# Optimization experiments

Measured on AMD Instinct MI355X. Metric: run time of the kernel, lower is better.

Reference implementation:

```python
import jax, jax.numpy as jnp
import numpy as np


def _unfold(x, k, pad, stride):
    # torch F.unfold: [B,C,H,W] -> [B, C*k*k, L] with (C, kh, kw) channel-major ordering
    B, C, H, W = x.shape
    xp = jnp.pad(x, ((0, 0), (0, 0), (pad, pad), (pad, pad)))
    oh = (H + 2 * pad - k) // stride + 1
    ow = (W + 2 * pad - k) // stride + 1
    rows = (jnp.arange(oh) * stride)[:, None] + jnp.arange(k)[None, :]  # [oh,k]
    cols = (jnp.arange(ow) * stride)[:, None] + jnp.arange(k)[None, :]  # [ow,k]
    p = xp[:, :, rows][:, :, :, :, cols]          # [B,C,oh,k,ow,k]
    p = p.transpose(0, 1, 3, 5, 2, 4)             # [B,C,k,k,oh,ow]
    return p.reshape(B, C * k * k, oh * ow)


def _fold(p, out_hw, k, pad, stride):
    # torch F.fold: overlap-add of patches [B, C*k*k, L] -> [B,C,H,W]
    B = p.shape[0]
    C = p.shape[1] // (k * k)
    H, W = out_hw
    oh = (H + 2 * pad - k) // stride + 1
    ow = (W + 2 * pad - k) // stride + 1
    p = p.reshape(B, C, k, k, oh, ow).transpose(0, 1, 4, 2, 5, 3)  # [B,C,oh,k,ow,k]
    rows = (jnp.arange(oh) * stride)[:, None] + jnp.arange(k)[None, :]  # [oh,k]
    cols = (jnp.arange(ow) * stride)[:, None] + jnp.arange(k)[None, :]  # [ow,k]
    out = jnp.zeros((B, C, H + 2 * pad, W + 2 * pad), p.dtype)
    out = out.at[:, :, rows[:, :, None, None], cols[None, None, :, :]].add(p)
    return out[:, :, pad:pad + H, pad:pad + W]


def _bis_gather(unf, idx):
    # torch.gather along dim=2 with per-batch index broadcast over channels
    return jnp.take_along_axis(unf, idx[:, None, :], axis=2)


def setup_inputs() -> dict:
    key = jax.random.key(0)
    k1, k2, k3, k4 = jax.random.split(key, 4)
    B, H, W = 4, 96, 96
    L = H * W
    return {
        "R_lv2_star_arg": jax.random.randint(k1, (B, L), 0, L, dtype=jnp.int64 if jax.config.jax_enable_x64 else jnp.int32).astype(jnp.int32),
        "lrsr_lv2": jax.random.normal(k2, (B, 64, H, W), dtype=jnp.float32),
        "ref_lv1": jax.random.normal(k3, (B, 64, 2 * H, 2 * W), dtype=jnp.float32),
        "ref_lv2": jax.random.normal(k4, (B, 128, H, W), dtype=jnp.float32),
    }


def reference(R_lv2_star_arg, lrsr_lv2, ref_lv1, ref_lv2):
    H, W = lrsr_lv2.shape[2], lrsr_lv2.shape[3]
    ref_lv2_unfold = _unfold(ref_lv2, 3, 1, 1)   # [B, C2*9, H*W]
    ref_lv1_unfold = _unfold(ref_lv1, 6, 2, 2)   # [B, C1*36, H*W]
    T_lv2_unfold = _bis_gather(ref_lv2_unfold, R_lv2_star_arg)
    T_lv1_unfold = _bis_gather(ref_lv1_unfold, R_lv2_star_arg)
    T_lv2 = _fold(T_lv2_unfold, (H, W), 3, 1, 1) / 9.0
    T_lv1 = _fold(T_lv1_unfold, (2 * H, 2 * W), 6, 2, 2) / 9.0
    return (T_lv2, T_lv1)
```

## Files before the change

kernel.cpp:

```cpp
#include <hip/hip_runtime.h>


typedef float f2 __attribute__((ext_vector_type(2)));
typedef float f4 __attribute__((ext_vector_type(4)));

#define NINE_INV (1.0f / 9.0f)
#define ZCELL 9216u

__device__ __forceinline__ unsigned cvt_pk_bf16(float a, float b) {
    unsigned r;
    asm("v_cvt_pk_bf16_f32 %0, %1, %2" : "=v"(r) : "v"(a), "v"(b));
    return r;
}
__device__ __forceinline__ f2 up2(unsigned w) {
    f2 r;
    r.x = __builtin_bit_cast(float, w << 16);
    r.y = __builtin_bit_cast(float, w & 0xffff0000u);
    return r;
}
template <typename T> __device__ __forceinline__ T ntload(const T* p) {
    return __builtin_nontemporal_load(p);
}
template <typename T> __device__ __forceinline__ void ntstore(T* p, T v) {
    __builtin_nontemporal_store(v, p);
}

__global__ __launch_bounds__(256) void table_kernel(
    const int* __restrict__ idx, uint4* __restrict__ tabA,
    unsigned short* __restrict__ tabB)
{
    int g = blockIdx.x * 256 + threadIdx.x;
    int b = g / 9216;
    int u = g - b * 9216;
    const int* idxb = idx + b * 9216;
    int r = u / 96, t = u - 96 * r;
    unsigned e[9];
#pragma unroll
    for (int i = 0; i < 3; ++i) {
        int oy = r - 1 + i;
        bool oyv = (unsigned)oy < 96u;
#pragma unroll
        for (int j = 0; j < 3; ++j) {
            int ox = t - 1 + j;
            bool pv = oyv & ((unsigned)ox < 96u);
            int jv = idxb[pv ? oy * 96 + ox : 0];
            int jy = jv / 96, jx = jv - 96 * jy;
            int ysh = jy + 1 - i, xsh = jx + 1 - j;
            bool sv = pv & ((unsigned)ysh < 96u) & ((unsigned)xsh < 96u);
            e[i * 3 + j] = sv ? (unsigned)(ysh * 96 + xsh) : ZCELL;
        }
    }
    uint4 w;
    w.x = e[0] | (e[1] << 16);
    w.y = e[2] | (e[3] << 16);
    w.z = e[4] | (e[5] << 16);
    w.w = e[6] | (e[7] << 16);
    tabA[g] = w;
    tabB[g] = (unsigned short)e[8];
}

template <bool TAB>
__global__ __launch_bounds__(512, 4) void transfer_kernel(
    const int* __restrict__ idx,
    const float* __restrict__ ref1,
    const float* __restrict__ ref2,
    const uint4* __restrict__ tabA,
    const unsigned short* __restrict__ tabB,
    float* __restrict__ out)
{
    __shared__ __align__(16) unsigned s2[18436];
    const int tid = threadIdx.x;
    const int bid = blockIdx.x;
    const int b = bid & 3;

    if (tid < 4) s2[18432 + tid] = 0;

    const uint4* tA = tabA + b * 9216;
    const unsigned short* tB = tabB + b * 9216;
    const int* idxb = idx + b * 9216;
    const f2 nv = {NINE_INV, NINE_INV};

    auto inline_cells = [&](int u, unsigned* e) {
        int r = u / 96, t = u - 96 * r;
#pragma unroll
        for (int i = 0; i < 3; ++i) {
            int oy = r - 1 + i;
            bool oyv = (unsigned)oy < 96u;
#pragma unroll
            for (int j = 0; j < 3; ++j) {
                int ox = t - 1 + j;
                bool pv = oyv & ((unsigned)ox < 96u);
                int jv = idxb[pv ? oy * 96 + ox : 0];
                int jy = jv / 96, jx = jv - 96 * jy;
                int ysh = jy + 1 - i, xsh = jx + 1 - j;
                bool sv = pv & ((unsigned)ysh < 96u) & ((unsigned)xsh < 96u);
                e[i * 3 + j] = sv ? (unsigned)(ysh * 96 + xsh) : ZCELL;
            }
        }
    };

    auto do_taps = [&](const unsigned* cw, unsigned c8, f2& a0, f2& a1) {
#pragma unroll
        for (int q = 0; q < 4; ++q) {
            unsigned lo = cw[q] & 0xffffu, hi = cw[q] >> 16;
            uint2 wa = *(const uint2*)((const char*)s2 + (lo << 3));
            uint2 wb = *(const uint2*)((const char*)s2 + (hi << 3));
            a0 += up2(wa.x); a1 += up2(wa.y);
            a0 += up2(wb.x); a1 += up2(wb.y);
        }
        uint2 wc = *(const uint2*)((const char*)s2 + (c8 << 3));
        a0 += up2(wc.x); a1 += up2(wc.y);
    };

    if (bid < 256) {
        const int q = (bid >> 2) & 1, c0 = (bid >> 3) * 2;
        const float* g0 = ref1 + (size_t)(b * 64 + c0) * 36864;

        for (int u2 = tid; u2 < 4608; u2 += 512) {
            int ysh = u2 / 48, xsh0 = 2 * (u2 - 48 * ysh);
            const float* gp = g0 + (size_t)(2 * ysh + q) * 192 + 2 * xsh0;
            f4 va = ntload((const f4*)gp);
            f4 vb = ntload((const f4*)(gp + 36864));
            uint4 w;
            w.x = cvt_pk_bf16(va.x, va.y); w.y = cvt_pk_bf16(vb.x, vb.y);
            w.z = cvt_pk_bf16(va.z, va.w); w.w = cvt_pk_bf16(vb.z, vb.w);
            *(uint4*)(s2 + 4 * u2) = w;
        }
        __syncthreads();

        float* ob = out + 4718592 + (size_t)(b * 64 + c0) * 36864;

        uint4 cA; unsigned cB;
        if (TAB) { cA = tA[tid]; cB = tB[tid]; }
        int u = tid;
#pragma unroll 2
        for (int k = 0; k < 18; ++k) {
            uint4 nA = cA; unsigned nB = cB;
            if (TAB && k < 17) { nA = tA[u + 512]; nB = tB[u + 512]; }
            unsigned cw[4];
            unsigned c8;
            if (TAB) {
                cw[0] = cA.x; cw[1] = cA.y; cw[2] = cA.z; cw[3] = cA.w; c8 = cB;
            } else {
                unsigned e[9];
                inline_cells(u, e);
                cw[0] = e[0] | (e[1] << 16); cw[1] = e[2] | (e[3] << 16);
                cw[2] = e[4] | (e[5] << 16); cw[3] = e[6] | (e[7] << 16);
                c8 = e[8];
            }
            f2 a0 = {0.f, 0.f}, a1 = {0.f, 0.f};
            do_taps(cw, c8, a0, a1);
            a0 *= nv; a1 *= nv;
            int r = u / 96, t = u - 96 * r;
            float* op = ob + (size_t)(2 * r + q) * 192 + 2 * t;
            ntstore((f2*)op, a0);
            ntstore((f2*)(op + 36864), a1);
            u += 512; cA = nA; cB = nB;
        }
    } else {
        const int r2 = bid - 256;
        const int grp = (r2 >> 2) & 31, h = (r2 >> 7) & 1;
        const int c0 = grp * 4;
        const float* g0 = ref2 + (size_t)(b * 128 + c0) * 9216;

        for (int u2 = tid; u2 < 4608; u2 += 512) {
            f2 p0 = ntload((const f2*)(g0 + 2 * u2));
            f2 p1 = ntload((const f2*)(g0 + 9216 + 2 * u2));
            f2 p2 = ntload((const f2*)(g0 + 2 * 9216 + 2 * u2));
            f2 p3 = ntload((const f2*)(g0 + 3 * 9216 + 2 * u2));
            uint4 w;
            w.x = cvt_pk_bf16(p0.x, p1.x); w.y = cvt_pk_bf16(p2.x, p3.x);
            w.z = cvt_pk_bf16(p0.y, p1.y); w.w = cvt_pk_bf16(p2.y, p3.y);
            *(uint4*)(s2 + 4 * u2) = w;
        }
        __syncthreads();

        float* ob = out + (size_t)(b * 128 + c0) * 9216;

        const int u0 = h * 4608;
        uint4 cA; unsigned cB;
        if (TAB) { cA = tA[u0 + tid]; cB = tB[u0 + tid]; }
        int u = u0 + tid;
#pragma unroll 2
        for (int k = 0; k < 9; ++k) {
            uint4 nA = cA; unsigned nB = cB;
            if (TAB && k < 8) { nA = tA[u + 512]; nB = tB[u + 512]; }
            unsigned cw[4];
            unsigned c8;
            if (TAB) {
                cw[0] = cA.x; cw[1] = cA.y; cw[2] = cA.z; cw[3] = cA.w; c8 = cB;
            } else {
                unsigned e[9];
                inline_cells(u, e);
                cw[0] = e[0] | (e[1] << 16); cw[1] = e[2] | (e[3] << 16);
                cw[2] = e[4] | (e[5] << 16); cw[3] = e[6] | (e[7] << 16);
                c8 = e[8];
            }
            f2 a0 = {0.f, 0.f}, a1 = {0.f, 0.f};
            do_taps(cw, c8, a0, a1);
            a0 *= nv; a1 *= nv;
            float* op = ob + u;
            ntstore(op, a0.x);            ntstore(op + 9216, a0.y);
            ntstore(op + 2 * 9216, a1.x); ntstore(op + 3 * 9216, a1.y);
            u += 512; cA = nA; cB = nB;
        }
    }
}

extern "C" void kernel_launch(void* const* d_in, const int* in_sizes, int n_in,
                              void* d_out, int out_size, void* d_ws, size_t ws_size,
                              hipStream_t stream) {
    const int*   idx  = (const int*)d_in[0];
    const float* ref1 = (const float*)d_in[2];
    const float* ref2 = (const float*)d_in[3];
    float* outp = (float*)d_out;

    uint4* tabA = (uint4*)d_ws;
    unsigned short* tabB = (unsigned short*)((char*)d_ws + (size_t)4 * 9216 * 16);

    const size_t need = (size_t)4 * 9216 * 16 + (size_t)4 * 9216 * 2;
    if (ws_size >= need) {
        hipLaunchKernelGGL(table_kernel, dim3(144), dim3(256), 0, stream,
                           idx, tabA, tabB);
        hipLaunchKernelGGL(transfer_kernel<true>, dim3(512), dim3(512), 0, stream,
                           idx, ref1, ref2, tabA, tabB, outp);
    } else {
        hipLaunchKernelGGL(transfer_kernel<false>, dim3(512), dim3(512), 0, stream,
                           idx, ref1, ref2, tabA, tabB, outp);
    }
}
```

Measured before the change: 27.69 us.

## Process more channels per block with wider LDS gathers and 1024-thread blocks

Each block now stages twice as many channels in shared memory (4 for the lv1 path, 8 for the lv2 path) as packed bf16, so one 16-byte LDS gather per tap serves more channels. The index-table reads per output position are therefore amortized over more channels. Blocks are doubled to 1024 threads, and the grid is halved to 256 blocks. The shared-memory footprint doubles to about 147KB per block, which limits blocks per CU, and the smaller grid may leave part of the GPU idle.

```diff
diff --git a/kernel.cpp b/kernel.cpp
--- a/kernel.cpp
+++ b/kernel.cpp
@@ -60,7 +60,7 @@
 }
 
 template <bool TAB>
-__global__ __launch_bounds__(512, 4) void transfer_kernel(
+__global__ __launch_bounds__(1024, 4) void transfer_kernel(
     const int* __restrict__ idx,
     const float* __restrict__ ref1,
     const float* __restrict__ ref2,
@@ -68,20 +68,21 @@
     const unsigned short* __restrict__ tabB,
     float* __restrict__ out)
 {
-    __shared__ __align__(16) unsigned s2[18436];
+    __shared__ __align__(16) unsigned s4[36868];
     const int tid = threadIdx.x;
     const int bid = blockIdx.x;
+
+    if (tid < 4) s4[36864 + tid] = 0;
+
     const int b = bid & 3;
-
-    if (tid < 4) s2[18432 + tid] = 0;
-
     const uint4* tA = tabA + b * 9216;
     const unsigned short* tB = tabB + b * 9216;
     const int* idxb = idx + b * 9216;
     const f2 nv = {NINE_INV, NINE_INV};
 
-    auto inline_cells = [&](int u, unsigned* e) {
+    auto make_cells = [&](int u, uint4& A, unsigned& B) {
         int r = u / 96, t = u - 96 * r;
+        unsigned e[9];
 #pragma unroll
         for (int i = 0; i < 3; ++i) {
             int oy = r - 1 + i;
@@ -97,34 +98,37 @@
                 e[i * 3 + j] = sv ? (unsigned)(ysh * 96 + xsh) : ZCELL;
             }
         }
+        A.x = e[0] | (e[1] << 16); A.y = e[2] | (e[3] << 16);
+        A.z = e[4] | (e[5] << 16); A.w = e[6] | (e[7] << 16);
+        B = e[8];
     };
 
-    auto do_taps = [&](const unsigned* cw, unsigned c8, f2& a0, f2& a1) {
-#pragma unroll
-        for (int q = 0; q < 4; ++q) {
-            unsigned lo = cw[q] & 0xffffu, hi = cw[q] >> 16;
-            uint2 wa = *(const uint2*)((const char*)s2 + (lo << 3));
-            uint2 wb = *(const uint2*)((const char*)s2 + (hi << 3));
-            a0 += up2(wa.x); a1 += up2(wa.y);
-            a0 += up2(wb.x); a1 += up2(wb.y);
-        }
-        uint2 wc = *(const uint2*)((const char*)s2 + (c8 << 3));
-        a0 += up2(wc.x); a1 += up2(wc.y);
+    auto gather4 = [&](uint4 cA, unsigned cB, f2& a0, f2& a1, f2& a2, f2& a3) {
+#define TAP(c) { uint4 w = *(const uint4*)((const char*)s4 + ((unsigned)(c) << 4)); \
+                 a0 += up2(w.x); a1 += up2(w.y); a2 += up2(w.z); a3 += up2(w.w); }
+        TAP(cA.x & 0xffffu); TAP(cA.x >> 16);
+        TAP(cA.y & 0xffffu); TAP(cA.y >> 16);
+        TAP(cA.z & 0xffffu); TAP(cA.z >> 16);
+        TAP(cA.w & 0xffffu); TAP(cA.w >> 16);
+        TAP(cB);
+#undef TAP
     };
 
-    if (bid < 256) {
-        const int q = (bid >> 2) & 1, c0 = (bid >> 3) * 2;
+    if (bid < 128) {
+        const int q = (bid >> 2) & 1, c0 = (bid >> 3) * 4;
         const float* g0 = ref1 + (size_t)(b * 64 + c0) * 36864;
 
-        for (int u2 = tid; u2 < 4608; u2 += 512) {
-            int ysh = u2 / 48, xsh0 = 2 * (u2 - 48 * ysh);
-            const float* gp = g0 + (size_t)(2 * ysh + q) * 192 + 2 * xsh0;
-            f4 va = ntload((const f4*)gp);
-            f4 vb = ntload((const f4*)(gp + 36864));
+        for (int u2 = tid; u2 < 9216; u2 += 1024) {
+            int ysh = u2 / 96, xsh = u2 - 96 * ysh;
+            const float* gp = g0 + (size_t)(2 * ysh + q) * 192 + 2 * xsh;
+            f2 v0 = ntload((const f2*)gp);
+            f2 v1 = ntload((const f2*)(gp + 36864));
+            f2 v2 = ntload((const f2*)(gp + 2 * 36864));
+            f2 v3 = ntload((const f2*)(gp + 3 * 36864));
             uint4 w;
-            w.x = cvt_pk_bf16(va.x, va.y); w.y = cvt_pk_bf16(vb.x, vb.y);
-            w.z = cvt_pk_bf16(va.z, va.w); w.w = cvt_pk_bf16(vb.z, vb.w);
-            *(uint4*)(s2 + 4 * u2) = w;
+            w.x = cvt_pk_bf16(v0.x, v0.y); w.y = cvt_pk_bf16(v1.x, v1.y);
+            w.z = cvt_pk_bf16(v2.x, v2.y); w.w = cvt_pk_bf16(v3.x, v3.y);
+            *(uint4*)(s4 + 4 * u2) = w;
         }
         __syncthreads();
 
@@ -134,75 +138,77 @@
         if (TAB) { cA = tA[tid]; cB = tB[tid]; }
         int u = tid;
 #pragma unroll 2
-        for (int k = 0; k < 18; ++k) {
+        for (int k = 0; k < 9; ++k) {
             uint4 nA = cA; unsigned nB = cB;
-            if (TAB && k < 17) { nA = tA[u + 512]; nB = tB[u + 512]; }
-            unsigned cw[4];
-            unsigned c8;
-            if (TAB) {
-                cw[0] = cA.x; cw[1] = cA.y; cw[2] = cA.z; cw[3] = cA.w; c8 = cB;
-            } else {
-                unsigned e[9];
-                inline_cells(u, e);
-                cw[0] = e[0] | (e[1] << 16); cw[1] = e[2] | (e[3] << 16);
-                cw[2] = e[4] | (e[5] << 16); cw[3] = e[6] | (e[7] << 16);
-                c8 = e[8];
-            }
-            f2 a0 = {0.f, 0.f}, a1 = {0.f, 0.f};
-            do_taps(cw, c8, a0, a1);
-            a0 *= nv; a1 *= nv;
+            if (TAB && k < 8) { nA = tA[u + 1024]; nB = tB[u + 1024]; }
+            if (!TAB) make_cells(u, cA, cB);
+            f2 a0 = {0.f, 0.f}, a1 = {0.f, 0.f}, a2 = {0.f, 0.f}, a3 = {0.f, 0.f};
+            gather4(cA, cB, a0, a1, a2, a3);
+            a0 *= nv; a1 *= nv; a2 *= nv; a3 *= nv;
             int r = u / 96, t = u - 96 * r;
             float* op = ob + (size_t)(2 * r + q) * 192 + 2 * t;
             ntstore((f2*)op, a0);
             ntstore((f2*)(op + 36864), a1);
-            u += 512; cA = nA; cB = nB;
+            ntstore((f2*)(op + 2 * 36864), a2);
+            ntstore((f2*)(op + 3 * 36864), a3);
+            u += 1024; cA = nA; cB = nB;
         }
     } else {
-        const int r2 = bid - 256;
-        const int grp = (r2 >> 2) & 31, h = (r2 >> 7) & 1;
-        const int c0 = grp * 4;
+        const int r2 = bid - 128;
+        const int grp = (r2 >> 2) & 15, h = (r2 >> 6) & 1;
+        const int c0 = grp * 8;
         const float* g0 = ref2 + (size_t)(b * 128 + c0) * 9216;
 
-        for (int u2 = tid; u2 < 4608; u2 += 512) {
-            f2 p0 = ntload((const f2*)(g0 + 2 * u2));
-            f2 p1 = ntload((const f2*)(g0 + 9216 + 2 * u2));
-            f2 p2 = ntload((const f2*)(g0 + 2 * 9216 + 2 * u2));
-            f2 p3 = ntload((const f2*)(g0 + 3 * 9216 + 2 * u2));
-            uint4 w;
-            w.x = cvt_pk_bf16(p0.x, p1.x); w.y = cvt_pk_bf16(p2.x, p3.x);
-            w.z = cvt_pk_bf16(p0.y, p1.y); w.w = cvt_pk_bf16(p2.y, p3.y);
-            *(uint4*)(s2 + 4 * u2) = w;
+        for (int p = tid; p < 4608; p += 1024) {
+            const float* gp = g0 + 2 * p;
+            f2 v0 = ntload((const f2*)gp);
+            f2 v1 = ntload((const f2*)(gp + 9216));
+            f2 v2 = ntload((const f2*)(gp + 2 * 9216));
+            f2 v3 = ntload((const f2*)(gp + 3 * 9216));
+            f2 v4 = ntload((const f2*)(gp + 4 * 9216));
+            f2 v5 = ntload((const f2*)(gp + 5 * 9216));
+            f2 v6 = ntload((const f2*)(gp + 6 * 9216));
+            f2 v7 = ntload((const f2*)(gp + 7 * 9216));
+            uint4 wa, wb;
+            wa.x = cvt_pk_bf16(v0.x, v1.x); wa.y = cvt_pk_bf16(v2.x, v3.x);
+            wa.z = cvt_pk_bf16(v4.x, v5.x); wa.w = cvt_pk_bf16(v6.x, v7.x);
+            wb.x = cvt_pk_bf16(v0.y, v1.y); wb.y = cvt_pk_bf16(v2.y, v3.y);
+            wb.z = cvt_pk_bf16(v4.y, v5.y); wb.w = cvt_pk_bf16(v6.y, v7.y);
+            *(uint4*)(s4 + 8 * p) = wa;
+            *(uint4*)(s4 + 8 * p + 4) = wb;
         }
         __syncthreads();
 
         float* ob = out + (size_t)(b * 128 + c0) * 9216;
-
         const int u0 = h * 4608;
-        uint4 cA; unsigned cB;
-        if (TAB) { cA = tA[u0 + tid]; cB = tB[u0 + tid]; }
-        int u = u0 + tid;
-#pragma unroll 2
-        for (int k = 0; k < 9; ++k) {
-            uint4 nA = cA; unsigned nB = cB;
-            if (TAB && k < 8) { nA = tA[u + 512]; nB = tB[u + 512]; }
-            unsigned cw[4];
-            unsigned c8;
-            if (TAB) {
-                cw[0] = cA.x; cw[1] = cA.y; cw[2] = cA.z; cw[3] = cA.w; c8 = cB;
-            } else {
-                unsigned e[9];
-                inline_cells(u, e);
-                cw[0] = e[0] | (e[1] << 16); cw[1] = e[2] | (e[3] << 16);
-                cw[2] = e[4] | (e[5] << 16); cw[3] = e[6] | (e[7] << 16);
-                c8 = e[8];
-            }
-            f2 a0 = {0.f, 0.f}, a1 = {0.f, 0.f};
-            do_taps(cw, c8, a0, a1);
-            a0 *= nv; a1 *= nv;
+
+        auto do_pos = [&](int u, uint4 cA, unsigned cB) {
+            f2 a0 = {0.f, 0.f}, a1 = {0.f, 0.f}, a2 = {0.f, 0.f}, a3 = {0.f, 0.f};
+            gather4(cA, cB, a0, a1, a2, a3);
+            a0 *= nv; a1 *= nv; a2 *= nv; a3 *= nv;
             float* op = ob + u;
             ntstore(op, a0.x);            ntstore(op + 9216, a0.y);
             ntstore(op + 2 * 9216, a1.x); ntstore(op + 3 * 9216, a1.y);
-            u += 512; cA = nA; cB = nB;
+            ntstore(op + 4 * 9216, a2.x); ntstore(op + 5 * 9216, a2.y);
+            ntstore(op + 6 * 9216, a3.x); ntstore(op + 7 * 9216, a3.y);
+        };
+
+        int u = u0 + tid;
+        uint4 cA; unsigned cB;
+        if (TAB) { cA = tA[u]; cB = tB[u]; }
+#pragma unroll
+        for (int k = 0; k < 4; ++k) {
+            bool has_next = (k < 3) | (tid < 512);
+            int un = has_next ? (u + 1024) : u;
+            uint4 nA = cA; unsigned nB = cB;
+            if (TAB) { nA = tA[un]; nB = tB[un]; }
+            if (!TAB) make_cells(u, cA, cB);
+            do_pos(u, cA, cB);
+            u = un; cA = nA; cB = nB;
+        }
+        if (tid < 512) {
+            if (!TAB) make_cells(u, cA, cB);
+            do_pos(u, cA, cB);
         }
     }
 }
@@ -222,10 +228,10 @@
     if (ws_size >= need) {
         hipLaunchKernelGGL(table_kernel, dim3(144), dim3(256), 0, stream,
                            idx, tabA, tabB);
-        hipLaunchKernelGGL(transfer_kernel<true>, dim3(512), dim3(512), 0, stream,
+        hipLaunchKernelGGL(transfer_kernel<true>, dim3(256), dim3(1024), 0, stream,
                            idx, ref1, ref2, tabA, tabB, outp);
     } else {
-        hipLaunchKernelGGL(transfer_kernel<false>, dim3(512), dim3(512), 0, stream,
+        hipLaunchKernelGGL(transfer_kernel<false>, dim3(256), dim3(1024), 0, stream,
                            idx, ref1, ref2, tabA, tabB, outp);
     }
 }
```

Result: slower. 31.03 us (+12.1%).
